# Kernel tuning notes

Hardware: AMD Instinct MI355X
Metric: run time of the kernel (lower is better)

Reference implementation:

```python
import jax, jax.numpy as jnp
import numpy as np

N, E, F_IN, H, OUT = 50000, 1600000, 128, 128, 32
NEG_SLOPE = 0.2


def setup_inputs() -> dict:
    key = jax.random.key(0)
    ks = jax.random.split(key, 9)
    s = lambda fan: 1.0 / np.sqrt(fan)
    x = jax.random.normal(ks[0], (N, F_IN), jnp.float32)
    edge_index = jax.random.randint(ks[1], (2, E), 0, N, jnp.int64)
    Wl1 = jax.random.normal(ks[2], (F_IN, H), jnp.float32) * s(F_IN)
    Wr1 = jax.random.normal(ks[3], (F_IN, H), jnp.float32) * s(F_IN)
    att1 = jax.random.normal(ks[4], (H,), jnp.float32) * s(H)
    b1 = jnp.zeros((H,), jnp.float32)
    Wl2 = jax.random.normal(ks[5], (H, OUT), jnp.float32) * s(H)
    Wr2 = jax.random.normal(ks[6], (H, OUT), jnp.float32) * s(H)
    att2 = jax.random.normal(ks[7], (OUT,), jnp.float32) * s(OUT)
    b2 = jnp.zeros((OUT,), jnp.float32)
    return {"x": x, "edge_index": edge_index, "Wl1": Wl1, "Wr1": Wr1,
            "att1": att1, "b1": b1, "Wl2": Wl2, "Wr2": Wr2, "att2": att2, "b2": b2}


def gatv2_layer(x, Wl, Wr, att, bias, src, dst, num_nodes):
    # PyG GATv2Conv (heads=1, concat=True, add_self_loops handled by caller)
    xl = x @ Wl  # source-side transform  [N, C]
    xr = x @ Wr  # target-side transform  [N, C]
    e = jax.nn.leaky_relu(xl[src] + xr[dst], NEG_SLOPE)  # [E, C]
    logits = e @ att  # [E]
    # segment softmax over incoming edges of each destination node
    m = jax.ops.segment_max(logits, dst, num_segments=num_nodes)  # [N]
    expv = jnp.exp(logits - m[dst])
    denom = jax.ops.segment_sum(expv, dst, num_segments=num_nodes)  # [N]
    alpha = expv / (denom[dst] + 1e-16)  # [E]
    out = jax.ops.segment_sum(xl[src] * alpha[:, None], dst, num_segments=num_nodes)
    return out + bias


def reference(x, edge_index, Wl1, Wr1, att1, b1, Wl2, Wr2, att2, b2):
    # add self-loops (PyG add_self_loops=True default)
    loops = jnp.arange(N, dtype=edge_index.dtype)
    src = jnp.concatenate([edge_index[0], loops])
    dst = jnp.concatenate([edge_index[1], loops])
    h = gatv2_layer(x, Wl1, Wr1, att1, b1, src, dst, N)
    h = jax.nn.relu(h)
    h = gatv2_layer(h, Wl2, Wr2, att2, b2, src, dst, N)
    return jax.nn.relu(h)
```

## Files before the change

kernel.cpp:

```cpp
#include <hip/hip_runtime.h>
#include <hip/hip_bf16.h>

#define N_NODES 50000
#define E_EDGES 1600000
#define E_TOT   (E_EDGES + N_NODES)
#define NEG_SLOPE 0.2f

#define NB       196
#define S1_TILE  4096
#define NT       ((E_TOT + S1_TILE - 1) / S1_TILE)
#define S2_CAP   10240

typedef _Float16 h2 __attribute__((ext_vector_type(2)));
typedef _Float16 h4 __attribute__((ext_vector_type(4)));
typedef _Float16 h8 __attribute__((ext_vector_type(8)));

__device__ __forceinline__ float fdot2h(h2 a, h2 b, float c)
{
#if __has_builtin(__builtin_amdgcn_fdot2)
    return __builtin_amdgcn_fdot2(a, b, c, false);
#else
    return c + (float)a[0] * (float)b[0] + (float)a[1] * (float)b[1];
#endif
}

__device__ __forceinline__ h2 habs2(h2 e)
{
    unsigned int u = __builtin_bit_cast(unsigned int, e) & 0x7FFF7FFFu;
    return __builtin_bit_cast(h2, u);
}

__device__ __forceinline__ int wave_iscan(int v, int lane)
{
#pragma unroll
    for (int off = 1; off < 64; off <<= 1) {
        int u = __shfl_up(v, off);
        if (lane >= off) v += u;
    }
    return v;
}

__global__ __launch_bounds__(256) void transform1_gemm(
    const float* __restrict__ x,
    const float* __restrict__ Wl, const float* __restrict__ Wr,
    _Float16* __restrict__ xl, _Float16* __restrict__ xr)
{
    __shared__ h2 xs2[16][128];
    __shared__ h2 ws2[16][128];
    const int n0 = blockIdx.x * 128;
    const float* __restrict__ W = blockIdx.y ? Wr : Wl;
    _Float16* __restrict__ Y = blockIdx.y ? xr : xl;
    const int t = threadIdx.x;
    const int tc = t & 15;
    const int tn = t >> 4;

    float acc[2][4][2][4];
#pragma unroll
    for (int nh = 0; nh < 2; ++nh)
#pragma unroll
        for (int i = 0; i < 4; ++i)
#pragma unroll
            for (int ch = 0; ch < 2; ++ch)
#pragma unroll
                for (int j = 0; j < 4; ++j) acc[nh][i][ch][j] = 0.f;

    for (int k0 = 0; k0 < 128; k0 += 32) {
        {
            const int node = t >> 1;
            const int kh = (t & 1) * 16;
            const int gn = n0 + node;
#pragma unroll
            for (int q = 0; q < 4; ++q) {
                float4 v = make_float4(0.f, 0.f, 0.f, 0.f);
                if (gn < N_NODES)
                    v = *(const float4*)&x[(size_t)gn * 128 + k0 + kh + q * 4];
                h2 p0 = {(_Float16)v.x, (_Float16)v.y};
                h2 p1 = {(_Float16)v.z, (_Float16)v.w};
                xs2[kh / 2 + q * 2 + 0][node] = p0;
                xs2[kh / 2 + q * 2 + 1][node] = p1;
            }
        }
        {
            const int c = t & 127;
            const int kq = (t >> 7) * 16;
#pragma unroll
            for (int ii = 0; ii < 8; ++ii) {
                h2 pw = {(_Float16)W[(size_t)(k0 + kq + 2 * ii) * 128 + c],
                         (_Float16)W[(size_t)(k0 + kq + 2 * ii + 1) * 128 + c]};
                ws2[kq / 2 + ii][c] = pw;
            }
        }
        __syncthreads();
#pragma unroll 4
        for (int k2 = 0; k2 < 16; ++k2) {
            h2 a0[4], a1[4], b0[4], b1[4];
#pragma unroll
            for (int j = 0; j < 4; ++j) {
                a0[j] = xs2[k2][tn * 4 + j];
                a1[j] = xs2[k2][64 + tn * 4 + j];
                b0[j] = ws2[k2][tc * 4 + j];
                b1[j] = ws2[k2][64 + tc * 4 + j];
            }
#pragma unroll
            for (int i = 0; i < 4; ++i)
#pragma unroll
                for (int j = 0; j < 4; ++j) {
                    acc[0][i][0][j] = fdot2h(a0[i], b0[j], acc[0][i][0][j]);
                    acc[0][i][1][j] = fdot2h(a0[i], b1[j], acc[0][i][1][j]);
                    acc[1][i][0][j] = fdot2h(a1[i], b0[j], acc[1][i][0][j]);
                    acc[1][i][1][j] = fdot2h(a1[i], b1[j], acc[1][i][1][j]);
                }
        }
        __syncthreads();
    }
#pragma unroll
    for (int nh = 0; nh < 2; ++nh)
#pragma unroll
        for (int i = 0; i < 4; ++i) {
            const int node = n0 + nh * 64 + tn * 4 + i;
            if (node < N_NODES) {
#pragma unroll
                for (int ch = 0; ch < 2; ++ch) {
                    h4 v;
                    v[0] = (_Float16)acc[nh][i][ch][0];
                    v[1] = (_Float16)acc[nh][i][ch][1];
                    v[2] = (_Float16)acc[nh][i][ch][2];
                    v[3] = (_Float16)acc[nh][i][ch][3];
                    *(h4*)&Y[(size_t)node * 128 + ch * 64 + tc * 4] = v;
                }
            }
        }
}

__global__ __launch_bounds__(256) void transform2_gemm(
    const _Float16* __restrict__ h,
    const float* __restrict__ Wl, const float* __restrict__ Wr,
    _Float16* __restrict__ hl, _Float16* __restrict__ hr)
{
    __shared__ h2 xs2[16][128];
    __shared__ h2 ws2[16][64];
    const int n0 = blockIdx.x * 128;
    const int t = threadIdx.x;
    const int tc = t & 15;
    const int tn = t >> 4;

    float acc[2][4][4];
#pragma unroll
    for (int nh = 0; nh < 2; ++nh)
#pragma unroll
        for (int i = 0; i < 4; ++i)
#pragma unroll
            for (int j = 0; j < 4; ++j) acc[nh][i][j] = 0.f;

    for (int k0 = 0; k0 < 128; k0 += 32) {
        {
            const int node = t >> 1;
            const int kh = (t & 1) * 16;
            const int gn = n0 + node;
            h8 v0 = {}, v1 = {};
            if (gn < N_NODES) {
                v0 = *(const h8*)&h[(size_t)gn * 128 + k0 + kh];
                v1 = *(const h8*)&h[(size_t)gn * 128 + k0 + kh + 8];
            }
#pragma unroll
            for (int q = 0; q < 4; ++q) {
                h2 p0 = {v0[2 * q], v0[2 * q + 1]};
                h2 p1 = {v1[2 * q], v1[2 * q + 1]};
                xs2[kh / 2 + q][node] = p0;
                xs2[kh / 2 + 4 + q][node] = p1;
            }
        }
        {
            const int c = t & 63;
            const int kq = (t >> 6) * 8;
            const float* __restrict__ Wm = (c < 32) ? Wl : Wr;
            const int wc = c & 31;
#pragma unroll
            for (int ii = 0; ii < 4; ++ii) {
                h2 pw = {(_Float16)Wm[(size_t)(k0 + kq + 2 * ii) * 32 + wc],
                         (_Float16)Wm[(size_t)(k0 + kq + 2 * ii + 1) * 32 + wc]};
                ws2[kq / 2 + ii][c] = pw;
            }
        }
        __syncthreads();
#pragma unroll 4
        for (int k2 = 0; k2 < 16; ++k2) {
            h2 a0[4], a1[4], b[4];
#pragma unroll
            for (int j = 0; j < 4; ++j) {
                a0[j] = xs2[k2][tn * 4 + j];
                a1[j] = xs2[k2][64 + tn * 4 + j];
                b[j] = ws2[k2][tc * 4 + j];
            }
#pragma unroll
            for (int i = 0; i < 4; ++i)
#pragma unroll
                for (int j = 0; j < 4; ++j) {
                    acc[0][i][j] = fdot2h(a0[i], b[j], acc[0][i][j]);
                    acc[1][i][j] = fdot2h(a1[i], b[j], acc[1][i][j]);
                }
        }
        __syncthreads();
    }
    _Float16* __restrict__ Y = (tc < 8) ? hl : hr;
    const int col = (tc < 8) ? tc * 4 : tc * 4 - 32;
#pragma unroll
    for (int nh = 0; nh < 2; ++nh)
#pragma unroll
        for (int i = 0; i < 4; ++i) {
            const int node = n0 + nh * 64 + tn * 4 + i;
            if (node < N_NODES) {
                h4 v;
                v[0] = (_Float16)acc[nh][i][0];
                v[1] = (_Float16)acc[nh][i][1];
                v[2] = (_Float16)acc[nh][i][2];
                v[3] = (_Float16)acc[nh][i][3];
                *(h4*)&Y[(size_t)node * 32 + col] = v;
            }
        }
}

__global__ __launch_bounds__(512) void tile_hist(
    const int* __restrict__ src, const int* __restrict__ dst,
    int* __restrict__ counts)
{
    __shared__ int hh[NB];
    const int t = threadIdx.x;
    const int base = blockIdx.x * S1_TILE;
    for (int i = t; i < NB; i += 512) hh[i] = 0;
    __syncthreads();
#pragma unroll
    for (int k = 0; k < S1_TILE / 512; ++k) {
        const int i = base + k * 512 + t;
        if (i < E_TOT) {
            const int d = (i < E_EDGES) ? dst[i] : (i - E_EDGES);
            atomicAdd(&hh[d >> 8], 1);
        }
    }
    __syncthreads();
    for (int b = t; b < NB; b += 512)
        counts[blockIdx.x * NB + b] = hh[b];
}

__global__ __launch_bounds__(512) void row_scan(
    const int* __restrict__ counts, int* __restrict__ rstart,
    int* __restrict__ bcount)
{
    __shared__ int wsum[8];
    const int b = blockIdx.x;
    const int t = threadIdx.x;
    const int lane = t & 63, wid = t >> 6;
    const int v = (t < NT) ? counts[t * NB + b] : 0;
    int inc = wave_iscan(v, lane);
    if (lane == 63) wsum[wid] = inc;
    __syncthreads();
    if (t == 0) {
        int s = 0;
#pragma unroll
        for (int w = 0; w < 8; ++w) { int u = wsum[w]; wsum[w] = s; s += u; }
    }
    __syncthreads();
    const int excl = inc - v + wsum[wid];
    if (t < NT) rstart[b * NT + t] = excl;
    if (t == 511) bcount[b] = excl;
}

__global__ __launch_bounds__(256) void bucket_base(
    const int* __restrict__ bcount, int* __restrict__ bbase)
{
    __shared__ int wsum[4];
    const int t = threadIdx.x;
    const int lane = t & 63, wid = t >> 6;
    int v = (t < NB) ? bcount[t] : 0;
    int inc = wave_iscan(v, lane);
    if (lane == 63) wsum[wid] = inc;
    __syncthreads();
    if (t == 0) {
        int s = 0;
#pragma unroll
        for (int w = 0; w < 4; ++w) { int u = wsum[w]; wsum[w] = s; s += u; }
    }
    __syncthreads();
    const int excl = inc - v + wsum[wid];
    if (t < NB) bbase[t] = excl;
    if (t == NB - 1) bbase[NB] = excl + v;
}

__global__ __launch_bounds__(512) void tile_scatter(
    const int* __restrict__ src, const int* __restrict__ dst,
    const int* __restrict__ rstart, const int* __restrict__ bbase,
    unsigned int* __restrict__ bucket_data)
{
    __shared__ int hh[256];
    __shared__ int cur[NB];
    __shared__ int rs[NB];
    __shared__ int wsum[8];
    __shared__ unsigned int srt[S1_TILE];
    const int t = threadIdx.x;
    const int tile = blockIdx.x;
    const int base = tile * S1_TILE;
    const int tcount = min(S1_TILE, E_TOT - base);

    for (int i = t; i < 256; i += 512) hh[i] = 0;
    __syncthreads();

    int eb[S1_TILE / 512];
    unsigned int ee[S1_TILE / 512];
#pragma unroll
    for (int k = 0; k < S1_TILE / 512; ++k) {
        const int i = base + k * 512 + t;
        eb[k] = -1;
        if (i < E_TOT) {
            int s, d;
            if (i < E_EDGES) { s = src[i]; d = dst[i]; }
            else { s = i - E_EDGES; d = s; }
            const int b = d >> 8;
            eb[k] = b;
            ee[k] = ((unsigned)b << 24) | ((unsigned)(d & 255) << 16) | (unsigned)s;
            atomicAdd(&hh[b], 1);
        }
    }
    __syncthreads();
    {
        const int lane = t & 63, wid = t >> 6;
        const int v = (t < 256) ? hh[t] : 0;
        int inc = wave_iscan(v, lane);
        if (lane == 63 && wid < 4) wsum[wid] = inc;
        __syncthreads();
        if (t == 0) {
            int s = 0;
#pragma unroll
            for (int w = 0; w < 4; ++w) { int u = wsum[w]; wsum[w] = s; s += u; }
        }
        __syncthreads();
        if (t < NB) {
            const int excl = inc - v + wsum[wid];
            cur[t] = excl;
            rs[t] = bbase[t] + rstart[t * NT + tile] - excl;
        }
    }
    __syncthreads();
#pragma unroll
    for (int k = 0; k < S1_TILE / 512; ++k) {
        if (eb[k] >= 0) {
            const int pos = atomicAdd(&cur[eb[k]], 1);
            srt[pos] = ee[k];
        }
    }
    __syncthreads();
    for (int i = t; i < tcount; i += 512) {
        const unsigned int e = srt[i];
        bucket_data[rs[e >> 24] + i] = e;
    }
}

__global__ __launch_bounds__(1024) void bucket_sort(
    const unsigned int* __restrict__ bucket_data,
    const int* __restrict__ bbase,
    int* __restrict__ offs, unsigned short* __restrict__ sorted_src)
{
    __shared__ int hist[256];
    __shared__ int hsrc[256];
    __shared__ int cur[256];
    __shared__ int csrc[256];
    __shared__ int wsum[4];
    __shared__ unsigned int srt4[S2_CAP];
    __shared__ unsigned short srt2[S2_CAP];
    const int b = blockIdx.x;
    const int t = threadIdx.x;
    const int lo = bbase[b], hi = bbase[b + 1];
    const int c = hi - lo;
    if (t < 256) { hist[t] = 0; hsrc[t] = 0; }
    __syncthreads();
    for (int i = t; i < c; i += 1024) {
        const unsigned int e = bucket_data[lo + i];
        atomicAdd(&hist[(e >> 16) & 255u], 1);
        atomicAdd(&hsrc[(e >> 8) & 255u], 1);
    }
    __syncthreads();
    {
        const int lane = t & 63, wid = t >> 6;
        const int v = (t < 256) ? hsrc[t] : 0;
        int inc = wave_iscan(v, lane);
        if (lane == 63 && wid < 4) wsum[wid] = inc;
        __syncthreads();
        if (t == 0) {
            int s = 0;
#pragma unroll
            for (int w = 0; w < 4; ++w) { int u = wsum[w]; wsum[w] = s; s += u; }
        }
        __syncthreads();
        if (t < 256) csrc[t] = inc - v + wsum[wid];
        __syncthreads();
    }
    {
        const int lane = t & 63, wid = t >> 6;
        const int v = (t < 256) ? hist[t] : 0;
        int inc = wave_iscan(v, lane);
        if (lane == 63 && wid < 4) wsum[wid] = inc;
        __syncthreads();
        if (t == 0) {
            int s = 0;
#pragma unroll
            for (int w = 0; w < 4; ++w) { int u = wsum[w]; wsum[w] = s; s += u; }
        }
        __syncthreads();
        if (t < 256) {
            const int excl = inc - v + wsum[wid];
            cur[t] = excl;
            const int node = b * 256 + t;
            if (node < N_NODES) offs[node] = lo + excl;
        }
    }
    if (b == 0 && t == 0) offs[N_NODES] = E_TOT;
    __syncthreads();
    for (int i = t; i < c; i += 1024) {
        const unsigned int e = bucket_data[lo + i];
        const int pos = atomicAdd(&csrc[(e >> 8) & 255u], 1);
        srt4[pos] = e;
    }
    __syncthreads();
    for (int i = t; i < c; i += 1024) {
        const unsigned int e = srt4[i];
        const int pos = atomicAdd(&cur[(e >> 16) & 255u], 1);
        srt2[pos] = (unsigned short)(e & 0xFFFFu);
    }
    __syncthreads();
    for (int i = t; i < c; i += 1024)
        sorted_src[lo + i] = srt2[i];
}

template <int C, int LPG, typename OUT_T>
__global__ __launch_bounds__(256) void gat_edge_pass(
    const _Float16* __restrict__ xl, const _Float16* __restrict__ xr,
    const float* __restrict__ att, const float* __restrict__ bias,
    const int* __restrict__ offs, const unsigned short* __restrict__ ssrc,
    OUT_T* __restrict__ out)
{
    constexpr int GPB = 256 / LPG;
    static_assert(C == LPG * 8, "8 halves per lane");
    const int node = blockIdx.x * GPB + threadIdx.x / LPG;
    if (node >= N_NODES) return;
    const int lane = threadIdx.x % LPG;
    const int cb = lane * 8;

    h2 a6[4], a4[4], r2[4];
    {
        const h8 rv = *(const h8*)(xr + (size_t)node * C + cb);
#pragma unroll
        for (int i = 0; i < 4; ++i) {
            const float av0 = att[cb + 2 * i], av1 = att[cb + 2 * i + 1];
            h2 t6 = {(_Float16)(0.6f * av0), (_Float16)(0.6f * av1)};
            h2 t4 = {(_Float16)(0.4f * av0), (_Float16)(0.4f * av1)};
            a6[i] = t6; a4[i] = t4;
            h2 rr = {rv[2 * i], rv[2 * i + 1]};
            r2[i] = rr;
        }
    }
    float acc[8];
#pragma unroll
    for (int v = 0; v < 8; ++v) acc[v] = 0.f;
    float m = -3.0e38f, denom = 0.f;

    const int p1 = offs[node + 1];
    int p = offs[node];

    for (; p + 4 <= p1; p += 4) {
        const int s0 = ssrc[p], s1 = ssrc[p + 1];
        const int s2 = ssrc[p + 2], s3 = ssrc[p + 3];
        const h8 x0 = *(const h8*)(xl + (size_t)s0 * C + cb);
        const h8 x1 = *(const h8*)(xl + (size_t)s1 * C + cb);
        const h8 x2 = *(const h8*)(xl + (size_t)s2 * C + cb);
        const h8 x3 = *(const h8*)(xl + (size_t)s3 * C + cb);
        float d0 = 0.f, d1 = 0.f, d2 = 0.f, d3 = 0.f;
#pragma unroll
        for (int i = 0; i < 4; ++i) {
            h2 xa = {x0[2 * i], x0[2 * i + 1]};
            h2 xb = {x1[2 * i], x1[2 * i + 1]};
            h2 xc = {x2[2 * i], x2[2 * i + 1]};
            h2 xd = {x3[2 * i], x3[2 * i + 1]};
            h2 e0 = xa + r2[i], e1 = xb + r2[i];
            h2 e2 = xc + r2[i], e3 = xd + r2[i];
            d0 = fdot2h(a6[i], e0, fdot2h(a4[i], habs2(e0), d0));
            d1 = fdot2h(a6[i], e1, fdot2h(a4[i], habs2(e1), d1));
            d2 = fdot2h(a6[i], e2, fdot2h(a4[i], habs2(e2), d2));
            d3 = fdot2h(a6[i], e3, fdot2h(a4[i], habs2(e3), d3));
        }
#pragma unroll
        for (int off = LPG >> 1; off; off >>= 1) {
            d0 += __shfl_xor(d0, off);
            d1 += __shfl_xor(d1, off);
            d2 += __shfl_xor(d2, off);
            d3 += __shfl_xor(d3, off);
        }
        const float pm = fmaxf(fmaxf(d0, d1), fmaxf(d2, d3));
        if (__builtin_expect(pm > m + 8.f, 0)) {
            const float sc = __expf(m - pm);
            m = pm;
            denom *= sc;
#pragma unroll
            for (int v = 0; v < 8; ++v) acc[v] *= sc;
        }
        const float w0 = __expf(d0 - m), w1 = __expf(d1 - m);
        const float w2 = __expf(d2 - m), w3 = __expf(d3 - m);
        denom += (w0 + w1) + (w2 + w3);
        const h2 wA = {(_Float16)w0, (_Float16)w1};
        const h2 wB = {(_Float16)w2, (_Float16)w3};
#pragma unroll
        for (int v = 0; v < 8; ++v) {
            h2 pA = {x0[v], x1[v]};
            h2 pB = {x2[v], x3[v]};
            acc[v] = fdot2h(wA, pA, fdot2h(wB, pB, acc[v]));
        }
    }
    for (; p + 2 <= p1; p += 2) {
        const int s0 = ssrc[p], s1 = ssrc[p + 1];
        const h8 x0 = *(const h8*)(xl + (size_t)s0 * C + cb);
        const h8 x1 = *(const h8*)(xl + (size_t)s1 * C + cb);
        float d0 = 0.f, d1 = 0.f;
#pragma unroll
        for (int i = 0; i < 4; ++i) {
            h2 xa = {x0[2 * i], x0[2 * i + 1]};
            h2 xb = {x1[2 * i], x1[2 * i + 1]};
            h2 e0 = xa + r2[i], e1 = xb + r2[i];
            d0 = fdot2h(a6[i], e0, fdot2h(a4[i], habs2(e0), d0));
            d1 = fdot2h(a6[i], e1, fdot2h(a4[i], habs2(e1), d1));
        }
#pragma unroll
        for (int off = LPG >> 1; off; off >>= 1) {
            d0 += __shfl_xor(d0, off);
            d1 += __shfl_xor(d1, off);
        }
        const float pm = fmaxf(d0, d1);
        if (__builtin_expect(pm > m + 8.f, 0)) {
            const float sc = __expf(m - pm);
            m = pm;
            denom *= sc;
#pragma unroll
            for (int v = 0; v < 8; ++v) acc[v] *= sc;
        }
        const float w0 = __expf(d0 - m), w1 = __expf(d1 - m);
        denom += w0 + w1;
        const h2 wA = {(_Float16)w0, (_Float16)w1};
#pragma unroll
        for (int v = 0; v < 8; ++v) {
            h2 pA = {x0[v], x1[v]};
            acc[v] = fdot2h(wA, pA, acc[v]);
        }
    }
    if (p < p1) {
        const int s0 = ssrc[p];
        const h8 x0 = *(const h8*)(xl + (size_t)s0 * C + cb);
        float d0 = 0.f;
#pragma unroll
        for (int i = 0; i < 4; ++i) {
            h2 xa = {x0[2 * i], x0[2 * i + 1]};
            h2 e0 = xa + r2[i];
            d0 = fdot2h(a6[i], e0, fdot2h(a4[i], habs2(e0), d0));
        }
#pragma unroll
        for (int off = LPG >> 1; off; off >>= 1) d0 += __shfl_xor(d0, off);
        if (d0 > m + 8.f) {
            const float sc = __expf(m - d0);
            m = d0;
            denom *= sc;
#pragma unroll
            for (int v = 0; v < 8; ++v) acc[v] *= sc;
        }
        const float w0 = __expf(d0 - m);
        denom += w0;
        const h2 wA = {(_Float16)w0, (_Float16)0.f};
#pragma unroll
        for (int v = 0; v < 8; ++v) {
            h2 pA = {x0[v], x0[v]};
            acc[v] = fdot2h(wA, pA, acc[v]);
        }
    }

    const float inv = 1.f / (denom + 1e-16f);
    if constexpr (sizeof(OUT_T) == 2) {
        h8 o;
#pragma unroll
        for (int v = 0; v < 8; ++v)
            o[v] = (_Float16)fmaxf(fmaf(acc[v], inv, bias[cb + v]), 0.f);
        *(h8*)&out[(size_t)node * C + cb] = o;
    } else {
        float4 o0, o1;
        o0.x = fmaxf(fmaf(acc[0], inv, bias[cb + 0]), 0.f);
        o0.y = fmaxf(fmaf(acc[1], inv, bias[cb + 1]), 0.f);
        o0.z = fmaxf(fmaf(acc[2], inv, bias[cb + 2]), 0.f);
        o0.w = fmaxf(fmaf(acc[3], inv, bias[cb + 3]), 0.f);
        o1.x = fmaxf(fmaf(acc[4], inv, bias[cb + 4]), 0.f);
        o1.y = fmaxf(fmaf(acc[5], inv, bias[cb + 5]), 0.f);
        o1.z = fmaxf(fmaf(acc[6], inv, bias[cb + 6]), 0.f);
        o1.w = fmaxf(fmaf(acc[7], inv, bias[cb + 7]), 0.f);
        *(float4*)&out[(size_t)node * C + cb] = o0;
        *(float4*)&out[(size_t)node * C + cb + 4] = o1;
    }
}

extern "C" void kernel_launch(void* const* d_in, const int* in_sizes, int n_in,
                              void* d_out, int out_size, void* d_ws, size_t ws_size,
                              hipStream_t stream)
{
    const float* x    = (const float*)d_in[0];
    const int*   ei   = (const int*)d_in[1];
    const float* Wl1  = (const float*)d_in[2];
    const float* Wr1  = (const float*)d_in[3];
    const float* att1 = (const float*)d_in[4];
    const float* b1   = (const float*)d_in[5];
    const float* Wl2  = (const float*)d_in[6];
    const float* Wr2  = (const float*)d_in[7];
    const float* att2 = (const float*)d_in[8];
    const float* b2   = (const float*)d_in[9];
    float* out = (float*)d_out;

    const int* e_src = ei;
    const int* e_dst = ei + E_EDGES;

    char* ws = (char*)d_ws;
    _Float16* xl = (_Float16*)(ws + 0);
    _Float16* xr = (_Float16*)(ws + 25600000);
    _Float16* h  = (_Float16*)(ws + 51200000);
    unsigned short* sorted_src = (unsigned short*)(ws + 76800000);
    int* offs   = (int*)(ws + 83400192);
    int* bbase  = (int*)(ws + 83600384);
    int* bcount = (int*)(ws + 83602432);
    unsigned int* bucket_data = (unsigned int*)(ws + 51200000);
    int* counts = (int*)(ws + 58000000);
    int* rstart = (int*)(ws + 58400000);
    _Float16* hl = xl;
    _Float16* hr = xr;

    transform1_gemm<<<dim3((N_NODES + 127) / 128, 2), 256, 0, stream>>>(
        x, Wl1, Wr1, xl, xr);

    tile_hist<<<NT, 512, 0, stream>>>(e_src, e_dst, counts);
    row_scan<<<NB, 512, 0, stream>>>(counts, rstart, bcount);
    bucket_base<<<1, 256, 0, stream>>>(bcount, bbase);
    tile_scatter<<<NT, 512, 0, stream>>>(e_src, e_dst, rstart, bbase, bucket_data);
    bucket_sort<<<NB, 1024, 0, stream>>>(bucket_data, bbase, offs, sorted_src);

    gat_edge_pass<128, 16, _Float16><<<N_NODES * 16 / 256, 256, 0, stream>>>(
        xl, xr, att1, b1, offs, sorted_src, h);

    transform2_gemm<<<(N_NODES + 127) / 128, 256, 0, stream>>>(
        h, Wl2, Wr2, hl, hr);

    gat_edge_pass<32, 4, float><<<(N_NODES * 4 + 255) / 256, 256, 0, stream>>>(
        hl, hr, att2, b2, offs, sorted_src, out);
}
```

Before: 166.5 us.

## Fuse GEMM with histogram, merge scans, and degree-sort nodes for edge pass

Merges the first transform GEMM and the edge-destination histogram into one launch using block-index partitioning. Folds the bucket-base scan into the row-scan kernel with a last-block-done atomic counter. Adds a per-bucket counting sort of nodes by in-degree, producing a permutation that the edge-pass kernels use so neighbouring groups handle nodes of similar degree. This cuts launch overhead and load imbalance, at the cost of an indirection load and extra shared-memory work in the bucket sort.

```diff
diff --git a/kernel.cpp b/kernel.cpp
--- a/kernel.cpp
+++ b/kernel.cpp
@@ -10,6 +10,7 @@
 #define S1_TILE  4096
 #define NT       ((E_TOT + S1_TILE - 1) / S1_TILE)
 #define S2_CAP   10240
+#define GB1      ((N_NODES + 127) / 128)
 
 typedef _Float16 h2 __attribute__((ext_vector_type(2)));
 typedef _Float16 h4 __attribute__((ext_vector_type(4)));
@@ -40,17 +41,41 @@
     return v;
 }
 
-__global__ __launch_bounds__(256) void transform1_gemm(
+__global__ __launch_bounds__(256) void fused_t1_hist(
     const float* __restrict__ x,
     const float* __restrict__ Wl, const float* __restrict__ Wr,
-    _Float16* __restrict__ xl, _Float16* __restrict__ xr)
+    _Float16* __restrict__ xl, _Float16* __restrict__ xr,
+    const int* __restrict__ src, const int* __restrict__ dst,
+    int* __restrict__ counts, int* __restrict__ done)
 {
     __shared__ h2 xs2[16][128];
     __shared__ h2 ws2[16][128];
-    const int n0 = blockIdx.x * 128;
-    const float* __restrict__ W = blockIdx.y ? Wr : Wl;
-    _Float16* __restrict__ Y = blockIdx.y ? xr : xl;
+    __shared__ int hh[NB];
     const int t = threadIdx.x;
+
+    if (blockIdx.x >= 2 * GB1) {
+        const int tile = blockIdx.x - 2 * GB1;
+        if (tile == 0 && t == 0) *done = 0;
+        const int base = tile * S1_TILE;
+        for (int i = t; i < NB; i += 256) hh[i] = 0;
+        __syncthreads();
+#pragma unroll
+        for (int k = 0; k < S1_TILE / 256; ++k) {
+            const int i = base + k * 256 + t;
+            if (i < E_TOT) {
+                const int d = (i < E_EDGES) ? dst[i] : (i - E_EDGES);
+                atomicAdd(&hh[d >> 8], 1);
+            }
+        }
+        __syncthreads();
+        for (int b = t; b < NB; b += 256)
+            counts[tile * NB + b] = hh[b];
+        return;
+    }
+
+    const int n0 = (blockIdx.x >> 1) * 128;
+    const float* __restrict__ W = (blockIdx.x & 1) ? Wr : Wl;
+    _Float16* __restrict__ Y = (blockIdx.x & 1) ? xr : xl;
     const int tc = t & 15;
     const int tn = t >> 4;
 
@@ -220,33 +245,12 @@
         }
 }
 
-__global__ __launch_bounds__(512) void tile_hist(
-    const int* __restrict__ src, const int* __restrict__ dst,
-    int* __restrict__ counts)
-{
-    __shared__ int hh[NB];
-    const int t = threadIdx.x;
-    const int base = blockIdx.x * S1_TILE;
-    for (int i = t; i < NB; i += 512) hh[i] = 0;
-    __syncthreads();
-#pragma unroll
-    for (int k = 0; k < S1_TILE / 512; ++k) {
-        const int i = base + k * 512 + t;
-        if (i < E_TOT) {
-            const int d = (i < E_EDGES) ? dst[i] : (i - E_EDGES);
-            atomicAdd(&hh[d >> 8], 1);
-        }
-    }
-    __syncthreads();
-    for (int b = t; b < NB; b += 512)
-        counts[blockIdx.x * NB + b] = hh[b];
-}
-
-__global__ __launch_bounds__(512) void row_scan(
+__global__ __launch_bounds__(512) void row_scan_base(
     const int* __restrict__ counts, int* __restrict__ rstart,
-    int* __restrict__ bcount)
+    int* __restrict__ bcount, int* __restrict__ bbase, int* __restrict__ done)
 {
     __shared__ int wsum[8];
+    __shared__ int amLast;
     const int b = blockIdx.x;
     const int t = threadIdx.x;
     const int lane = t & 63, wid = t >> 6;
@@ -262,28 +266,31 @@
     __syncthreads();
     const int excl = inc - v + wsum[wid];
     if (t < NT) rstart[b * NT + t] = excl;
-    if (t == 511) bcount[b] = excl;
-}
-
-__global__ __launch_bounds__(256) void bucket_base(
-    const int* __restrict__ bcount, int* __restrict__ bbase)
-{
-    __shared__ int wsum[4];
-    const int t = threadIdx.x;
-    const int lane = t & 63, wid = t >> 6;
-    int v = (t < NB) ? bcount[t] : 0;
-    int inc = wave_iscan(v, lane);
-    if (lane == 63) wsum[wid] = inc;
-    __syncthreads();
-    if (t == 0) {
-        int s = 0;
-#pragma unroll
-        for (int w = 0; w < 4; ++w) { int u = wsum[w]; wsum[w] = s; s += u; }
-    }
-    __syncthreads();
-    const int excl = inc - v + wsum[wid];
-    if (t < NB) bbase[t] = excl;
-    if (t == NB - 1) bbase[NB] = excl + v;
+    if (t == 511) {
+        bcount[b] = excl;
+        __threadfence();
+        const int old = atomicAdd(done, 1);
+        amLast = (old == NB - 1) ? 1 : 0;
+    }
+    __syncthreads();
+    if (amLast) {
+        __threadfence();
+        const int v2 = (t < NB) ? bcount[t] : 0;
+        int inc2 = wave_iscan(v2, lane);
+        if (lane == 63 && wid < 4) wsum[wid] = inc2;
+        __syncthreads();
+        if (t == 0) {
+            int s = 0;
+#pragma unroll
+            for (int w = 0; w < 4; ++w) { int u = wsum[w]; wsum[w] = s; s += u; }
+        }
+        __syncthreads();
+        if (t < 256) {
+            const int excl2 = inc2 - v2 + wsum[wid];
+            if (t < NB) bbase[t] = excl2;
+            if (t == NB - 1) bbase[NB] = excl2 + v2;
+        }
+    }
 }
 
 __global__ __launch_bounds__(512) void tile_scatter(
@@ -357,12 +364,14 @@
 __global__ __launch_bounds__(1024) void bucket_sort(
     const unsigned int* __restrict__ bucket_data,
     const int* __restrict__ bbase,
-    int* __restrict__ offs, unsigned short* __restrict__ sorted_src)
+    int* __restrict__ offs, unsigned short* __restrict__ sorted_src,
+    unsigned short* __restrict__ perm)
 {
     __shared__ int hist[256];
     __shared__ int hsrc[256];
     __shared__ int cur[256];
     __shared__ int csrc[256];
+    __shared__ int dcur[256];
     __shared__ int wsum[4];
     __shared__ unsigned int srt4[S2_CAP];
     __shared__ unsigned short srt2[S2_CAP];
@@ -370,7 +379,7 @@
     const int t = threadIdx.x;
     const int lo = bbase[b], hi = bbase[b + 1];
     const int c = hi - lo;
-    if (t < 256) { hist[t] = 0; hsrc[t] = 0; }
+    if (t < 256) { hist[t] = 0; hsrc[t] = 0; dcur[t] = 0; }
     __syncthreads();
     for (int i = t; i < c; i += 1024) {
         const unsigned int e = bucket_data[lo + i];
@@ -378,6 +387,31 @@
         atomicAdd(&hsrc[(e >> 8) & 255u], 1);
     }
     __syncthreads();
+    const bool valid = (t < 256) && (b * 256 + t < N_NODES);
+    const int mydeg = valid ? min(hist[t], 255) : 0;
+    if (valid) atomicAdd(&dcur[mydeg], 1);
+    __syncthreads();
+    {
+        const int lane = t & 63, wid = t >> 6;
+        const int v = (t < 256) ? dcur[t] : 0;
+        int inc = wave_iscan(v, lane);
+        if (lane == 63 && wid < 4) wsum[wid] = inc;
+        __syncthreads();
+        if (t == 0) {
+            int s = 0;
+#pragma unroll
+            for (int w = 0; w < 4; ++w) { int u = wsum[w]; wsum[w] = s; s += u; }
+        }
+        __syncthreads();
+        const int excl = inc - v + wsum[wid];
+        __syncthreads();
+        if (t < 256) dcur[t] = excl;
+        __syncthreads();
+    }
+    if (valid) {
+        const int rank = atomicAdd(&dcur[mydeg], 1);
+        perm[b * 256 + rank] = (unsigned short)(b * 256 + t);
+    }
     {
         const int lane = t & 63, wid = t >> 6;
         const int v = (t < 256) ? hsrc[t] : 0;
@@ -435,12 +469,14 @@
     const _Float16* __restrict__ xl, const _Float16* __restrict__ xr,
     const float* __restrict__ att, const float* __restrict__ bias,
     const int* __restrict__ offs, const unsigned short* __restrict__ ssrc,
+    const unsigned short* __restrict__ perm,
     OUT_T* __restrict__ out)
 {
     constexpr int GPB = 256 / LPG;
     static_assert(C == LPG * 8, "8 halves per lane");
-    const int node = blockIdx.x * GPB + threadIdx.x / LPG;
-    if (node >= N_NODES) return;
+    const int gid = blockIdx.x * GPB + threadIdx.x / LPG;
+    if (gid >= N_NODES) return;
+    const int node = perm[gid];
     const int lane = threadIdx.x % LPG;
     const int cb = lane * 8;
 
@@ -626,27 +662,29 @@
     int* offs   = (int*)(ws + 83400192);
     int* bbase  = (int*)(ws + 83600384);
     int* bcount = (int*)(ws + 83602432);
+    unsigned short* perm = (unsigned short*)(ws + 83603456);
+    int* done   = (int*)(ws + 83703808);
     unsigned int* bucket_data = (unsigned int*)(ws + 51200000);
     int* counts = (int*)(ws + 58000000);
     int* rstart = (int*)(ws + 58400000);
     _Float16* hl = xl;
     _Float16* hr = xr;
 
-    transform1_gemm<<<dim3((N_NODES + 127) / 128, 2), 256, 0, stream>>>(
-        x, Wl1, Wr1, xl, xr);
-
-    tile_hist<<<NT, 512, 0, stream>>>(e_src, e_dst, counts);
-    row_scan<<<NB, 512, 0, stream>>>(counts, rstart, bcount);
-    bucket_base<<<1, 256, 0, stream>>>(bcount, bbase);
+    fused_t1_hist<<<2 * GB1 + NT, 256, 0, stream>>>(
+        x, Wl1, Wr1, xl, xr, e_src, e_dst, counts, done);
+
+    row_scan_base<<<NB, 512, 0, stream>>>(counts, rstart, bcount, bbase, done);
+
     tile_scatter<<<NT, 512, 0, stream>>>(e_src, e_dst, rstart, bbase, bucket_data);
-    bucket_sort<<<NB, 1024, 0, stream>>>(bucket_data, bbase, offs, sorted_src);
+
+    bucket_sort<<<NB, 1024, 0, stream>>>(bucket_data, bbase, offs, sorted_src, perm);
 
     gat_edge_pass<128, 16, _Float16><<<N_NODES * 16 / 256, 256, 0, stream>>>(
-        xl, xr, att1, b1, offs, sorted_src, h);
+        xl, xr, att1, b1, offs, sorted_src, perm, h);
 
     transform2_gemm<<<(N_NODES + 127) / 128, 256, 0, stream>>>(
         h, Wl2, Wr2, hl, hr);
 
     gat_edge_pass<32, 4, float><<<(N_NODES * 4 + 255) / 256, 256, 0, stream>>>(
-        hl, hr, att2, b2, offs, sorted_src, out);
-}
+        hl, hr, att2, b2, offs, sorted_src, perm, out);
+}
```

Result: slower. 171.5 us (+3.0%).
